# Kernel tuning notes

Measured on AMD Instinct MI355X. Metric: run time of the kernel, lower is better.

The kernel has to match this reference:

```python
import jax, jax.numpy as jnp
import numpy as np

B, S, K, V, H = 32, 2048, 512, 512, 256


def setup_inputs() -> dict:
    key = jax.random.key(0)
    ks = jax.random.split(key, 6)
    r = 0.1  # init_range
    return {
        "q": jax.random.normal(ks[0], (B, K), jnp.float32),
        "k": jax.random.normal(ks[1], (S, B, K), jnp.float32),
        "v": jax.random.normal(ks[2], (S, B, V), jnp.float32),
        "Wk": jax.random.uniform(ks[3], (H, K), jnp.float32, -r, r),
        "bk": jnp.zeros((H,), jnp.float32),
        "Wq": jax.random.uniform(ks[4], (H, K), jnp.float32, -r, r),
        "bq": jnp.zeros((H,), jnp.float32),
        "Wo": jax.random.uniform(ks[5], (1, H), jnp.float32, -r, r),
        "bo": jnp.zeros((1,), jnp.float32),
    }


def reference(q, k, v, Wk, bk, Wq, bq, Wo, bo):
    # k, v: [S, B, *] -> batch-first [B, S, *]
    kb = jnp.transpose(k, (1, 0, 2))  # [B, S, K]
    vb = jnp.transpose(v, (1, 0, 2))  # [B, S, V]
    h_k = jnp.einsum('bsk,hk->bsh', kb, Wk) + bk        # key2hid
    h_q = q @ Wq.T + bq                                  # [B, H]
    h = jnp.tanh(h_k + h_q[:, None, :])                  # [B, S, H]
    logit = jnp.einsum('bsh,h->bs', h, Wo[0]) + bo[0]    # hid2output, squeeze
    logit = logit - jnp.max(logit, axis=1, keepdims=True)
    p = jax.nn.softmax(logit, axis=1)                    # [B, S]
    out = jnp.sum(vb * p[:, :, None], axis=1, keepdims=True)  # [B, 1, V]
    out = jnp.transpose(out, (1, 0, 2))                  # [1, B, V]
    return out, p
```

## Files before the change

kernel.cpp:

```cpp
#include <hip/hip_runtime.h>
#include <stdint.h>

#define Bb 32
#define Ss 2048
#define Kk 512
#define Vv 512
#define Hh 256

#define OUTP (Bb * Vv)

#define WS_HQ 0
#define WS_WKB 32768
#define WS_LOGIT 294912

typedef float floatx4 __attribute__((ext_vector_type(4)));
typedef __bf16 bf16x8 __attribute__((ext_vector_type(8)));

__device__ __forceinline__ uint32_t bfround(float f) {
  uint32_t u = __float_as_uint(f);
  return (u + 0x7fffu + ((u >> 16) & 1u)) >> 16;
}
__device__ __forceinline__ uint32_t packbf(float lo, float hi) {
  return bfround(lo) | (bfround(hi) << 16);
}

__device__ __forceinline__ void gload_lds16(const uint16_t* g, uint16_t* l) {
  __builtin_amdgcn_global_load_lds((const __attribute__((address_space(1))) void*)g,
                                   (__attribute__((address_space(3))) void*)l, 16, 0, 0);
}

__global__ void prep(const float* __restrict__ q, const float* __restrict__ Wq,
                     const float* __restrict__ bq, const float* __restrict__ bk,
                     const float* __restrict__ Wk, uint16_t* __restrict__ wkb,
                     float* __restrict__ hq) {
  __shared__ float red[256];
  const int bx = blockIdx.x;
  const int t = threadIdx.x;
  if (bx < 128) {
    const int i = (bx * 256 + t) * 4;
    float4 w = *(const float4*)(Wk + i);
    const int h = i >> 9;
    const int k = i & 511;
    const int stage = k >> 6;
    const int kin = k & 63;
    const int grp = kin >> 3;
    const int j = kin & 7;
    uint2 pk;
    pk.x = packbf(w.x, w.y);
    pk.y = packbf(w.z, w.w);
    *(uint2*)(wkb + stage * 16384 + (grp * 256 + h) * 8 + j) = pk;
  } else {
    const int idx = bx - 128;
    const int b = idx >> 3;
    const int hc = idx & 7;
    const int h_in = t & 31;
    const int kp = t >> 5;
    const int h = hc * 32 + h_in;
    const float4* qp = (const float4*)(q + b * Kk + kp * 64);
    const float4* wp = (const float4*)(Wq + h * Kk + kp * 64);
    float acc = 0.f;
#pragma unroll
    for (int i = 0; i < 16; ++i) {
      float4 qa = qp[i], wa = wp[i];
      acc = fmaf(qa.x, wa.x, acc);
      acc = fmaf(qa.y, wa.y, acc);
      acc = fmaf(qa.z, wa.z, acc);
      acc = fmaf(qa.w, wa.w, acc);
    }
    red[t] = acc;
    __syncthreads();
    if (t < 32) {
      float s = 0.f;
#pragma unroll
      for (int kp2 = 0; kp2 < 8; ++kp2) s += red[kp2 * 32 + t];
      const int hh = hc * 32 + t;
      hq[b * Hh + hh] = s + bq[hh] + bk[hh];
    }
  }
}

__global__ __launch_bounds__(256, 3) void fused_gemm_tanh_logit(
    const float* __restrict__ kin, const uint16_t* __restrict__ wkb,
    const float* __restrict__ hq, const float* __restrict__ Wo,
    float* __restrict__ logits) {
  __shared__ __align__(16) uint16_t lA[64 * 64];
  __shared__ __align__(16) uint16_t lB[256 * 64];
  __shared__ float lpart[4][64];

  const int tid = threadIdx.x;
  const int b = blockIdx.y;
  const int s0 = blockIdx.x * 64;
  const int wid = tid >> 6;
  const int lane = tid & 63;
  const int l15 = lane & 15;
  const int lg = lane >> 4;

  float hqv[4], wov[4];
#pragma unroll
  for (int ni = 0; ni < 4; ++ni) {
    const int n = wid * 64 + ni * 16 + l15;
    hqv[ni] = hq[b * Hh + n];
    wov[ni] = Wo[n];
  }

  floatx4 acc[4][4];
#pragma unroll
  for (int mi = 0; mi < 4; ++mi)
#pragma unroll
    for (int ni = 0; ni < 4; ++ni) acc[mi][ni] = (floatx4){0.f, 0.f, 0.f, 0.f};

  const int kg = tid >> 5;
  const int mrow = (tid & 31) * 2;
  const float* a0 = kin + ((size_t)(s0 + mrow) * Bb + b) * Kk + kg * 8;
  const float* a1 = a0 + (size_t)Bb * Kk;

  float4 av0, av1, av2, av3;
  av0 = *(const float4*)(a0);
  av1 = *(const float4*)(a0 + 4);
  av2 = *(const float4*)(a1);
  av3 = *(const float4*)(a1 + 4);

  const uint16_t* bstage = wkb + (wid * 8) * 512 + lane * 8;
  uint16_t* bdst0 = &lB[(wid * 8) * 512];

  for (int ks = 0; ks < 8; ++ks) {
    __syncthreads();
    uint4 w0, w1;
    w0.x = packbf(av0.x, av0.y);
    w0.y = packbf(av0.z, av0.w);
    w0.z = packbf(av1.x, av1.y);
    w0.w = packbf(av1.z, av1.w);
    w1.x = packbf(av2.x, av2.y);
    w1.y = packbf(av2.z, av2.w);
    w1.z = packbf(av3.x, av3.y);
    w1.w = packbf(av3.z, av3.w);
    *(uint4*)&lA[(kg * 64 + mrow) * 8] = w0;
    *(uint4*)&lA[(kg * 64 + mrow + 1) * 8] = w1;
    const uint16_t* bsrc = bstage + ks * 16384;
#pragma unroll
    for (int it = 0; it < 8; ++it) gload_lds16(bsrc + it * 512, bdst0 + it * 512);
    __syncthreads();
    if (ks < 7) {
      av0 = *(const float4*)(a0 + (ks + 1) * 64);
      av1 = *(const float4*)(a0 + (ks + 1) * 64 + 4);
      av2 = *(const float4*)(a1 + (ks + 1) * 64);
      av3 = *(const float4*)(a1 + (ks + 1) * 64 + 4);
    }
#pragma unroll
    for (int kk = 0; kk < 2; ++kk) {
      bf16x8 af[4], bfr[4];
#pragma unroll
      for (int mi = 0; mi < 4; ++mi)
        af[mi] = *(const bf16x8*)&lA[((kk * 4 + lg) * 64 + mi * 16 + l15) * 8];
#pragma unroll
      for (int ni = 0; ni < 4; ++ni)
        bfr[ni] = *(const bf16x8*)&lB[((kk * 4 + lg) * 256 + wid * 64 + ni * 16 + l15) * 8];
#pragma unroll
      for (int mi = 0; mi < 4; ++mi)
#pragma unroll
        for (int ni = 0; ni < 4; ++ni)
          acc[mi][ni] =
              __builtin_amdgcn_mfma_f32_16x16x32_bf16(af[mi], bfr[ni], acc[mi][ni], 0, 0, 0);
    }
  }

#pragma unroll
  for (int mi = 0; mi < 4; ++mi) {
#pragma unroll
    for (int r = 0; r < 4; ++r) {
      float sum = 0.f;
#pragma unroll
      for (int ni = 0; ni < 4; ++ni) {
        const float x = acc[mi][ni][r] + hqv[ni];
        const float e = __expf(2.f * x);
        const float th = 1.f - 2.f * __builtin_amdgcn_rcpf(e + 1.f);
        sum = fmaf(th, wov[ni], sum);
      }
      sum += __shfl_xor(sum, 1, 64);
      sum += __shfl_xor(sum, 2, 64);
      sum += __shfl_xor(sum, 4, 64);
      sum += __shfl_xor(sum, 8, 64);
      if (l15 == 0) lpart[wid][mi * 16 + lg * 4 + r] = sum;
    }
  }
  __syncthreads();
  if (tid < 64) {
    const float lv = lpart[0][tid] + lpart[1][tid] + lpart[2][tid] + lpart[3][tid];
    logits[b * Ss + s0 + tid] = lv;
  }
}

__global__ void softmax_zero(const float* __restrict__ logits, float* __restrict__ dout) {
  const int b = blockIdx.x;
  const int t = threadIdx.x;
  const int wid = t >> 6, lane = t & 63;
  __shared__ float red[4];
  const float4* lp = (const float4*)(logits + b * Ss);
  const float4 x0 = lp[t * 2], x1 = lp[t * 2 + 1];
  float mx = fmaxf(fmaxf(fmaxf(x0.x, x0.y), fmaxf(x0.z, x0.w)),
                   fmaxf(fmaxf(x1.x, x1.y), fmaxf(x1.z, x1.w)));
#pragma unroll
  for (int off = 1; off < 64; off <<= 1) mx = fmaxf(mx, __shfl_xor(mx, off, 64));
  if (lane == 0) red[wid] = mx;
  __syncthreads();
  mx = fmaxf(fmaxf(red[0], red[1]), fmaxf(red[2], red[3]));
  __syncthreads();
  float e[8];
  e[0] = __expf(x0.x - mx); e[1] = __expf(x0.y - mx);
  e[2] = __expf(x0.z - mx); e[3] = __expf(x0.w - mx);
  e[4] = __expf(x1.x - mx); e[5] = __expf(x1.y - mx);
  e[6] = __expf(x1.z - mx); e[7] = __expf(x1.w - mx);
  float s = ((e[0] + e[1]) + (e[2] + e[3])) + ((e[4] + e[5]) + (e[6] + e[7]));
#pragma unroll
  for (int off = 1; off < 64; off <<= 1) s += __shfl_xor(s, off, 64);
  if (lane == 0) red[wid] = s;
  __syncthreads();
  s = (red[0] + red[1]) + (red[2] + red[3]);
  const float inv = 1.f / s;
  float4 p0, p1;
  p0.x = e[0] * inv; p0.y = e[1] * inv; p0.z = e[2] * inv; p0.w = e[3] * inv;
  p1.x = e[4] * inv; p1.y = e[5] * inv; p1.z = e[6] * inv; p1.w = e[7] * inv;
  float4* pout = (float4*)(dout + OUTP + b * Ss);
  pout[t * 2] = p0;
  pout[t * 2 + 1] = p1;
  dout[b * Vv + t] = 0.f;
  dout[b * Vv + 256 + t] = 0.f;
}

__global__ __launch_bounds__(256) void weighted_vsum(const float* __restrict__ v,
                                                     float* __restrict__ dout) {
  const int sc = blockIdx.x;
  const int b = blockIdx.y;
  const int t = threadIdx.x;
  __shared__ float lp[128];
  if (t < 128) lp[t] = dout[OUTP + b * Ss + sc * 128 + t];
  __syncthreads();
  const int c4 = t & 127;
  const int sh = t >> 7;
  float4 acc = {0.f, 0.f, 0.f, 0.f};
#pragma unroll 8
  for (int i = 0; i < 64; ++i) {
    const int sl = sh + 2 * i;
    const int s = sc * 128 + sl;
    const float4 vv = *(const float4*)(v + ((size_t)s * Bb + b) * Vv + c4 * 4);
    const float pw = lp[sl];
    acc.x = fmaf(pw, vv.x, acc.x);
    acc.y = fmaf(pw, vv.y, acc.y);
    acc.z = fmaf(pw, vv.z, acc.z);
    acc.w = fmaf(pw, vv.w, acc.w);
  }
  float* o = dout + b * Vv + c4 * 4;
  atomicAdd(o + 0, acc.x);
  atomicAdd(o + 1, acc.y);
  atomicAdd(o + 2, acc.z);
  atomicAdd(o + 3, acc.w);
}

extern "C" void kernel_launch(void* const* d_in, const int* in_sizes, int n_in,
                              void* d_out, int out_size, void* d_ws, size_t ws_size,
                              hipStream_t stream) {
  const float* q  = (const float*)d_in[0];
  const float* k  = (const float*)d_in[1];
  const float* v  = (const float*)d_in[2];
  const float* Wk = (const float*)d_in[3];
  const float* bk = (const float*)d_in[4];
  const float* Wq = (const float*)d_in[5];
  const float* bq = (const float*)d_in[6];
  const float* Wo = (const float*)d_in[7];

  float* out = (float*)d_out;
  char* ws = (char*)d_ws;
  float* hq = (float*)(ws + WS_HQ);
  uint16_t* wkb = (uint16_t*)(ws + WS_WKB);
  float* logits = (float*)(ws + WS_LOGIT);

  prep<<<dim3(384), dim3(256), 0, stream>>>(q, Wq, bq, bk, Wk, wkb, hq);
  fused_gemm_tanh_logit<<<dim3(Ss / 64, Bb), dim3(256), 0, stream>>>(k, wkb, hq, Wo, logits);
  softmax_zero<<<dim3(Bb), dim3(256), 0, stream>>>(logits, out);
  weighted_vsum<<<dim3(16, Bb), dim3(256), 0, stream>>>(v, out);
}
```

Measured before the change: 330.9 us.

## Double-buffer Wk tiles in LDS, coalesce k loads, split vsum over more blocks

The GEMM kernel now double-buffers the bf16 Wk tile in LDS and issues the next tile's async loads before the current MFMA step, so global latency overlaps compute. The k-tile loads are remapped so 16 threads read 64 contiguous floats per row, which coalesces better. Occupancy drops from 3 to 2 blocks per CU because of the extra LDS. weighted_vsum uses 32-row chunks with 64 blocks per batch, giving more parallelism at the cost of four times as many atomics.

```diff
diff --git a/kernel.cpp b/kernel.cpp
--- a/kernel.cpp
+++ b/kernel.cpp
@@ -79,12 +79,12 @@
   }
 }
 
-__global__ __launch_bounds__(256, 3) void fused_gemm_tanh_logit(
+__global__ __launch_bounds__(256, 2) void fused_gemm_tanh_logit(
     const float* __restrict__ kin, const uint16_t* __restrict__ wkb,
     const float* __restrict__ hq, const float* __restrict__ Wo,
     float* __restrict__ logits) {
   __shared__ __align__(16) uint16_t lA[64 * 64];
-  __shared__ __align__(16) uint16_t lB[256 * 64];
+  __shared__ __align__(16) uint16_t lB[2][256 * 64];
   __shared__ float lpart[4][64];
 
   const int tid = threadIdx.x;
@@ -95,6 +95,22 @@
   const int l15 = lane & 15;
   const int lg = lane >> 4;
 
+  const int r = tid >> 4;
+  const int c0 = (tid & 15) * 4;
+  const float* abase = kin + ((size_t)s0 * Bb + b) * Kk + c0;
+
+  float4 av[4];
+#pragma unroll
+  for (int it = 0; it < 4; ++it)
+    av[it] = *(const float4*)(abase + (size_t)(it * 16 + r) * (Bb * Kk));
+
+  const uint16_t* bsrc0 = wkb + wid * 4096 + lane * 8;
+  {
+    uint16_t* bd = &lB[0][wid * 4096];
+#pragma unroll
+    for (int it = 0; it < 8; ++it) gload_lds16(bsrc0 + it * 512, bd + it * 512);
+  }
+
   float hqv[4], wov[4];
 #pragma unroll
   for (int ni = 0; ni < 4; ++ni) {
@@ -109,43 +125,26 @@
 #pragma unroll
     for (int ni = 0; ni < 4; ++ni) acc[mi][ni] = (floatx4){0.f, 0.f, 0.f, 0.f};
 
-  const int kg = tid >> 5;
-  const int mrow = (tid & 31) * 2;
-  const float* a0 = kin + ((size_t)(s0 + mrow) * Bb + b) * Kk + kg * 8;
-  const float* a1 = a0 + (size_t)Bb * Kk;
-
-  float4 av0, av1, av2, av3;
-  av0 = *(const float4*)(a0);
-  av1 = *(const float4*)(a0 + 4);
-  av2 = *(const float4*)(a1);
-  av3 = *(const float4*)(a1 + 4);
-
-  const uint16_t* bstage = wkb + (wid * 8) * 512 + lane * 8;
-  uint16_t* bdst0 = &lB[(wid * 8) * 512];
-
   for (int ks = 0; ks < 8; ++ks) {
     __syncthreads();
-    uint4 w0, w1;
-    w0.x = packbf(av0.x, av0.y);
-    w0.y = packbf(av0.z, av0.w);
-    w0.z = packbf(av1.x, av1.y);
-    w0.w = packbf(av1.z, av1.w);
-    w1.x = packbf(av2.x, av2.y);
-    w1.y = packbf(av2.z, av2.w);
-    w1.z = packbf(av3.x, av3.y);
-    w1.w = packbf(av3.z, av3.w);
-    *(uint4*)&lA[(kg * 64 + mrow) * 8] = w0;
-    *(uint4*)&lA[(kg * 64 + mrow + 1) * 8] = w1;
-    const uint16_t* bsrc = bstage + ks * 16384;
-#pragma unroll
-    for (int it = 0; it < 8; ++it) gload_lds16(bsrc + it * 512, bdst0 + it * 512);
+#pragma unroll
+    for (int it = 0; it < 4; ++it) {
+      uint2 pk;
+      pk.x = packbf(av[it].x, av[it].y);
+      pk.y = packbf(av[it].z, av[it].w);
+      *(uint2*)&lA[((c0 >> 3) * 64 + it * 16 + r) * 8 + (c0 & 7)] = pk;
+    }
     __syncthreads();
     if (ks < 7) {
-      av0 = *(const float4*)(a0 + (ks + 1) * 64);
-      av1 = *(const float4*)(a0 + (ks + 1) * 64 + 4);
-      av2 = *(const float4*)(a1 + (ks + 1) * 64);
-      av3 = *(const float4*)(a1 + (ks + 1) * 64 + 4);
-    }
+      const uint16_t* bs = wkb + (ks + 1) * 16384 + wid * 4096 + lane * 8;
+      uint16_t* bd = &lB[(ks + 1) & 1][wid * 4096];
+#pragma unroll
+      for (int it = 0; it < 8; ++it) gload_lds16(bs + it * 512, bd + it * 512);
+#pragma unroll
+      for (int it = 0; it < 4; ++it)
+        av[it] = *(const float4*)(abase + (ks + 1) * 64 + (size_t)(it * 16 + r) * (Bb * Kk));
+    }
+    const uint16_t* lBc = lB[ks & 1];
 #pragma unroll
     for (int kk = 0; kk < 2; ++kk) {
       bf16x8 af[4], bfr[4];
@@ -154,7 +153,7 @@
         af[mi] = *(const bf16x8*)&lA[((kk * 4 + lg) * 64 + mi * 16 + l15) * 8];
 #pragma unroll
       for (int ni = 0; ni < 4; ++ni)
-        bfr[ni] = *(const bf16x8*)&lB[((kk * 4 + lg) * 256 + wid * 64 + ni * 16 + l15) * 8];
+        bfr[ni] = *(const bf16x8*)&lBc[((kk * 4 + lg) * 256 + wid * 64 + ni * 16 + l15) * 8];
 #pragma unroll
       for (int mi = 0; mi < 4; ++mi)
 #pragma unroll
@@ -167,11 +166,11 @@
 #pragma unroll
   for (int mi = 0; mi < 4; ++mi) {
 #pragma unroll
-    for (int r = 0; r < 4; ++r) {
+    for (int rr = 0; rr < 4; ++rr) {
       float sum = 0.f;
 #pragma unroll
       for (int ni = 0; ni < 4; ++ni) {
-        const float x = acc[mi][ni][r] + hqv[ni];
+        const float x = acc[mi][ni][rr] + hqv[ni];
         const float e = __expf(2.f * x);
         const float th = 1.f - 2.f * __builtin_amdgcn_rcpf(e + 1.f);
         sum = fmaf(th, wov[ni], sum);
@@ -180,7 +179,7 @@
       sum += __shfl_xor(sum, 2, 64);
       sum += __shfl_xor(sum, 4, 64);
       sum += __shfl_xor(sum, 8, 64);
-      if (l15 == 0) lpart[wid][mi * 16 + lg * 4 + r] = sum;
+      if (l15 == 0) lpart[wid][mi * 16 + lg * 4 + rr] = sum;
     }
   }
   __syncthreads();
@@ -232,16 +231,16 @@
   const int sc = blockIdx.x;
   const int b = blockIdx.y;
   const int t = threadIdx.x;
-  __shared__ float lp[128];
-  if (t < 128) lp[t] = dout[OUTP + b * Ss + sc * 128 + t];
+  __shared__ float lp[32];
+  if (t < 32) lp[t] = dout[OUTP + b * Ss + sc * 32 + t];
   __syncthreads();
   const int c4 = t & 127;
   const int sh = t >> 7;
   float4 acc = {0.f, 0.f, 0.f, 0.f};
-#pragma unroll 8
-  for (int i = 0; i < 64; ++i) {
+#pragma unroll
+  for (int i = 0; i < 16; ++i) {
     const int sl = sh + 2 * i;
-    const int s = sc * 128 + sl;
+    const int s = sc * 32 + sl;
     const float4 vv = *(const float4*)(v + ((size_t)s * Bb + b) * Vv + c4 * 4);
     const float pw = lp[sl];
     acc.x = fmaf(pw, vv.x, acc.x);
@@ -277,5 +276,5 @@
   prep<<<dim3(384), dim3(256), 0, stream>>>(q, Wq, bq, bk, Wk, wkb, hq);
   fused_gemm_tanh_logit<<<dim3(Ss / 64, Bb), dim3(256), 0, stream>>>(k, wkb, hq, Wo, logits);
   softmax_zero<<<dim3(Bb), dim3(256), 0, stream>>>(logits, out);
-  weighted_vsum<<<dim3(16, Bb), dim3(256), 0, stream>>>(v, out);
-}
+  weighted_vsum<<<dim3(64, Bb), dim3(256), 0, stream>>>(v, out);
+}
```

After: 333.0 us. No clear change (+0.6%).
